# Kernel tuning notes

Measured on AMD Instinct MI355X. Metric: run time of the kernel, lower is better.

Reference implementation:

```python
import jax, jax.numpy as jnp
import numpy as np

B, N, D, H = 32, 64, 128, 256
LN_EPS = 1e-5


def _mlp(x, W1, b1, g, beta, W2, b2):
    # Linear -> LayerNorm -> GELU (exact erf) -> Linear
    h = x @ W1 + b1
    mu = jnp.mean(h, axis=-1, keepdims=True)
    var = jnp.var(h, axis=-1, keepdims=True)
    h = (h - mu) * jax.lax.rsqrt(var + LN_EPS) * g + beta
    h = jax.nn.gelu(h, approximate=False)
    return h @ W2 + b2


def setup_inputs() -> dict:
    key = jax.random.key(0)
    ks = jax.random.split(key, 10)
    s = lambda fan_in: 1.0 / np.sqrt(fan_in)
    return {
        "slots": jax.random.normal(ks[0], (B, N, D), dtype=jnp.float32),
        "adjacency": jax.random.uniform(ks[1], (B, N, N), dtype=jnp.float32),
        # edge_net params
        "We1": jax.random.uniform(ks[2], (2 * D, H), minval=-s(2 * D), maxval=s(2 * D), dtype=jnp.float32),
        "be1": jnp.zeros((H,), jnp.float32),
        "ge": jnp.ones((H,), jnp.float32),
        "bge": jnp.zeros((H,), jnp.float32),
        "We2": jax.random.uniform(ks[3], (H, D), minval=-s(H), maxval=s(H), dtype=jnp.float32),
        "be2": jnp.zeros((D,), jnp.float32),
        # node_net params
        "Wn1": jax.random.uniform(ks[4], (2 * D, H), minval=-s(2 * D), maxval=s(2 * D), dtype=jnp.float32),
        "bn1": jnp.zeros((H,), jnp.float32),
        "gn": jnp.ones((H,), jnp.float32),
        "bgn": jnp.zeros((H,), jnp.float32),
        "Wn2": jax.random.uniform(ks[5], (H, D), minval=-s(H), maxval=s(H), dtype=jnp.float32),
        "bn2": jnp.zeros((D,), jnp.float32),
    }


def reference(slots, adjacency, We1, be1, ge, bge, We2, be2, Wn1, bn1, gn, bgn, Wn2, bn2):
    b, n, d = slots.shape
    # all-pairs edge features: receiver i, sender j -> [B,N,N,2D]
    ei = jnp.broadcast_to(slots[:, :, None, :], (b, n, n, d))
    ej = jnp.broadcast_to(slots[:, None, :, :], (b, n, n, d))
    edge_feat = jnp.concatenate([ei, ej], axis=-1)
    edge_out = _mlp(edge_feat, We1, be1, ge, bge, We2, be2)  # [B,N,N,D]
    # mask diagonal (i != j) and weight by adjacency, then reduce over j
    mask = 1.0 - jnp.eye(n, dtype=slots.dtype)
    w = adjacency * mask  # [B,N,N]
    messages = jnp.einsum('bij,bijd->bid', w, edge_out)
    node_input = jnp.concatenate([slots, messages], axis=-1)
    delta = _mlp(node_input, Wn1, bn1, gn, bgn, Wn2, bn2)
    return slots + delta
```

## Files before the change

### kernel.cpp

```cpp
#include <hip/hip_runtime.h>

#define NB 32
#define NN 64
#define ND 128
#define NH 256
#define LN_EPS 1e-5f
#define RP 4

typedef __attribute__((ext_vector_type(8))) short bf16x8;
typedef __attribute__((ext_vector_type(4))) float f32x4;

__device__ __forceinline__ float gelu2(float x) {
    const float au  = fabsf(x);
    const float xpa = x + au;
    const float z   = au * 0.70710678118654752440f;
    const float z2  = z * z;
    const float pc  = fmaf(0.078108f, z, 0.000972f);
    const float pb  = fmaf(0.278393f, z, 1.0f);
    const float p   = fmaf(z2, fmaf(z, pc, 0.230389f), pb);
    const float p2  = p * p;
    const float r   = __builtin_amdgcn_rcpf(p2 * p2);
    return fmaf(-au, r, xpa);
}
__device__ __forceinline__ float gelu_h(float x) { return 0.5f * gelu2(x); }

__device__ __forceinline__ short f2bf(float f) {
    unsigned u = __float_as_uint(f);
    u += 0x7FFFu + ((u >> 16) & 1u);
    return (short)(u >> 16);
}

__global__ __launch_bounds__(256) void k_pre(const float* __restrict__ slots,
                                             const float* __restrict__ We1,
                                             const float* __restrict__ be1,
                                             const float* __restrict__ Wn1,
                                             const float* __restrict__ We2,
                                             const float* __restrict__ be2,
                                             float* __restrict__ Pt,
                                             float* __restrict__ Qm,
                                             float* __restrict__ XW,
                                             short* __restrict__ Pb,
                                             short* __restrict__ Qb,
                                             float4* __restrict__ rowstats,
                                             float* __restrict__ WC,
                                             float* __restrict__ v) {
    __shared__ float xs[RP][ND];
    __shared__ float red[4][RP][4];
    const int t = threadIdx.x;

    if (blockIdx.x >= 512) {
        const int bid2 = blockIdx.x - 512;
        if (bid2 == 64) {
            __shared__ float bs[ND];
            if (t < ND) bs[t] = be2[t];
            __syncthreads();
            float acc = 0.f;
            #pragma unroll 4
            for (int d = 0; d < ND; ++d) acc = fmaf(bs[d], Wn1[(ND + d) * NH + t], acc);
            v[t] = acc;
            return;
        }
        const int k0 = bid2 * 4;
        __shared__ float ws[4][ND];
        #pragma unroll
        for (int i = 0; i < 2; ++i) {
            const int idx = t + i * 256;
            ws[idx >> 7][idx & 127] = We2[(k0 + (idx >> 7)) * ND + (idx & 127)];
        }
        __syncthreads();
        float acc[4] = {0.f, 0.f, 0.f, 0.f};
        #pragma unroll 4
        for (int d = 0; d < ND; ++d) {
            const float wn = Wn1[(ND + d) * NH + t];
            #pragma unroll
            for (int r = 0; r < 4; ++r) acc[r] = fmaf(ws[r][d], wn, acc[r]);
        }
        #pragma unroll
        for (int r = 0; r < 4; ++r) WC[(k0 + r) * NH + t] = acc[r];
        return;
    }

    const int r0 = blockIdx.x * RP;
    const int lane = t & 63, wave = t >> 6;
    #pragma unroll
    for (int i = 0; i < 2; ++i) {
        const int idx = t + i * 256;
        xs[idx >> 7][idx & 127] = slots[(size_t)(r0 + (idx >> 7)) * ND + (idx & 127)];
    }
    __syncthreads();
    float pt[RP], qq[RP], xw[RP];
    const float bb = be1[t];
    #pragma unroll
    for (int r = 0; r < RP; ++r) { pt[r] = bb; qq[r] = 0.f; xw[r] = 0.f; }
    #pragma unroll 4
    for (int d = 0; d < ND; ++d) {
        const float wt  = We1[d * NH + t];
        const float wbt = We1[(ND + d) * NH + t];
        const float wn  = Wn1[d * NH + t];
        #pragma unroll
        for (int r = 0; r < RP; ++r) {
            const float x = xs[r][d];
            pt[r] = fmaf(x, wt,  pt[r]);
            qq[r] = fmaf(x, wbt, qq[r]);
            xw[r] = fmaf(x, wn,  xw[r]);
        }
    }
    #pragma unroll
    for (int r = 0; r < RP; ++r) {
        const size_t row = (size_t)(r0 + r);
        Pt[row * NH + t] = pt[r];
        Qm[row * NH + t] = qq[r];
        XW[row * NH + t] = xw[r];
        Pb[row * NH + t] = f2bf(pt[r]);
        Qb[row * NH + t] = f2bf(qq[r]);
    }
    float s1[RP], s2[RP], s3[RP], s4[RP];
    #pragma unroll
    for (int r = 0; r < RP; ++r) {
        s1[r] = pt[r]; s2[r] = pt[r] * pt[r];
        s3[r] = qq[r]; s4[r] = qq[r] * qq[r];
    }
    #pragma unroll
    for (int off = 32; off; off >>= 1) {
        #pragma unroll
        for (int r = 0; r < RP; ++r) {
            s1[r] += __shfl_xor(s1[r], off);
            s2[r] += __shfl_xor(s2[r], off);
            s3[r] += __shfl_xor(s3[r], off);
            s4[r] += __shfl_xor(s4[r], off);
        }
    }
    if (lane == 0) {
        #pragma unroll
        for (int r = 0; r < RP; ++r) {
            red[wave][r][0] = s1[r]; red[wave][r][1] = s2[r];
            red[wave][r][2] = s3[r]; red[wave][r][3] = s4[r];
        }
    }
    __syncthreads();
    if (t < RP) {
        float4 st;
        st.x = (red[0][t][0] + red[1][t][0]) + (red[2][t][0] + red[3][t][0]);
        st.y = (red[0][t][1] + red[1][t][1]) + (red[2][t][1] + red[3][t][1]);
        st.z = (red[0][t][2] + red[1][t][2]) + (red[2][t][2] + red[3][t][2]);
        st.w = (red[0][t][3] + red[1][t][3]) + (red[2][t][3] + red[3][t][3]);
        rowstats[r0 + t] = st;
    }
}

__global__ __launch_bounds__(256) void k_dot(
    const short* __restrict__ Pb, const short* __restrict__ Qb,
    const float4* __restrict__ rowstats,
    const float* __restrict__ adj,
    float4* __restrict__ wmrG)
{
    const int b  = blockIdx.x >> 2;
    const int jt = blockIdx.x & 3;
    const int t  = threadIdx.x;
    const int l  = t & 63;
    const int i0 = (t >> 6) * 16;
    const int j0 = jt * 16;
    const int rA = l & 15;
    const int kg = l >> 4;

    const short* Prow = Pb + ((size_t)b * NN + i0 + rA) * NH + kg * 8;
    const short* Qrow = Qb + ((size_t)b * NN + j0 + rA) * NH + kg * 8;
    f32x4 acc = {0.f, 0.f, 0.f, 0.f};
    #pragma unroll
    for (int kc = 0; kc < 8; ++kc) {
        const bf16x8 av = *(const bf16x8*)(Prow + kc * 32);
        const bf16x8 bv = *(const bf16x8*)(Qrow + kc * 32);
        acc = __builtin_amdgcn_mfma_f32_16x16x32_bf16(av, bv, acc, 0, 0, 0);
    }
    const int j  = j0 + (l & 15);
    const int gj = b * NN + j;
    const float4 stj = rowstats[gj];
    const float inv = 1.0f / NH;
    #pragma unroll
    for (int q = 0; q < 4; ++q) {
        const int i  = i0 + (l >> 4) * 4 + q;
        const int gi = b * NN + i;
        const float4 sti = rowstats[gi];
        float a = adj[(size_t)gi * NN + j];
        if (j == i) a = 0.f;
        const float cd = acc[q];
        const float mu = (sti.x + stj.z) * inv;
        const float e2 = fmaf(2.f, cd, sti.y + stj.w) * inv;
        const float rr = __builtin_amdgcn_rsqf(fmaf(-mu, mu, e2) + LN_EPS);
        wmrG[(size_t)gi * NN + j] = make_float4(0.5f * a, rr, -mu * rr, a);
    }
}

__global__ __launch_bounds__(256, 4) void k_mn(
    const float* __restrict__ slots,
    const float* __restrict__ Pt,
    const float* __restrict__ Qm,
    const float4* __restrict__ wmrG,
    const float* __restrict__ ge,  const float* __restrict__ bge,
    const float* __restrict__ XW,
    const float* __restrict__ WC, const float* __restrict__ v,
    const float* __restrict__ bn1,
    const float* __restrict__ gn,  const float* __restrict__ bgn,
    const float* __restrict__ Wn2, const float* __restrict__ bn2,
    float* __restrict__ out)
{
    union U {
        struct { float4 wmr[2][NN]; float s[4][2][NH]; } e;
        struct { float sfg[2][NH];
                 union { float part[2][4][NH]; float d[2][8][ND + 4]; } w; } n;
    };
    __shared__ U u;
    __shared__ float lds_ws[2];
    __shared__ float lds_red[4][2][2];
    __shared__ float lds_mr[2][2];

    const int row0 = blockIdx.x * 2;
    const int b    = row0 >> 6;
    const int t    = threadIdx.x;
    const int lane = t & 63;
    const int wave = t >> 6;

    const float xw0 = XW[(size_t)row0 * NH + t];
    const float xw1 = XW[(size_t)(row0 + 1) * NH + t];
    const float sl  = slots[(size_t)(row0 + (t >> 7)) * ND + (t & 127)];
    if (t < 128) {
        const int r = t >> 6, j = t & 63;
        u.e.wmr[r][j] = wmrG[(size_t)(row0 + r) * NN + j];
    }
    const float4 P0 = ((const float4*)(Pt + (size_t)row0 * NH))[lane];
    const float4 P1 = ((const float4*)(Pt + (size_t)(row0 + 1) * NH))[lane];
    const float4 G  = ((const float4*)ge)[lane];
    const float4 Bg = ((const float4*)bge)[lane];
    __syncthreads();

    if (wave < 2) {
        float wv = u.e.wmr[wave][lane].w;
        #pragma unroll
        for (int off = 32; off; off >>= 1) wv += __shfl_xor(wv, off);
        if (lane == 0) lds_ws[wave] = wv;
    }

    const float4* Qb4 = (const float4*)(Qm + (size_t)b * NN * NH) + lane;
    float4 A0 = make_float4(0.f, 0.f, 0.f, 0.f);
    float4 A1 = make_float4(0.f, 0.f, 0.f, 0.f);
    #pragma unroll 4
    for (int k = 0; k < 16; ++k) {
        const int jj = wave + 4 * k;
        const float4 q  = Qb4[jj * (NH / 4)];
        const float4 m0 = u.e.wmr[0][jj];
        const float4 m1 = u.e.wmr[1][jj];
        float h, uu;
        h = P0.x + q.x; uu = fmaf(fmaf(h, m0.y, m0.z), G.x, Bg.x); A0.x = fmaf(m0.x, gelu2(uu), A0.x);
        h = P0.y + q.y; uu = fmaf(fmaf(h, m0.y, m0.z), G.y, Bg.y); A0.y = fmaf(m0.x, gelu2(uu), A0.y);
        h = P0.z + q.z; uu = fmaf(fmaf(h, m0.y, m0.z), G.z, Bg.z); A0.z = fmaf(m0.x, gelu2(uu), A0.z);
        h = P0.w + q.w; uu = fmaf(fmaf(h, m0.y, m0.z), G.w, Bg.w); A0.w = fmaf(m0.x, gelu2(uu), A0.w);
        h = P1.x + q.x; uu = fmaf(fmaf(h, m1.y, m1.z), G.x, Bg.x); A1.x = fmaf(m1.x, gelu2(uu), A1.x);
        h = P1.y + q.y; uu = fmaf(fmaf(h, m1.y, m1.z), G.y, Bg.y); A1.y = fmaf(m1.x, gelu2(uu), A1.y);
        h = P1.z + q.z; uu = fmaf(fmaf(h, m1.y, m1.z), G.z, Bg.z); A1.z = fmaf(m1.x, gelu2(uu), A1.z);
        h = P1.w + q.w; uu = fmaf(fmaf(h, m1.y, m1.z), G.w, Bg.w); A1.w = fmaf(m1.x, gelu2(uu), A1.w);
    }
    ((float4*)u.e.s[wave][0])[lane] = A0;
    ((float4*)u.e.s[wave][1])[lane] = A1;
    __syncthreads();

    const float sf0 = (u.e.s[0][0][t] + u.e.s[1][0][t]) + (u.e.s[2][0][t] + u.e.s[3][0][t]);
    const float sf1 = (u.e.s[0][1][t] + u.e.s[1][1][t]) + (u.e.s[2][1][t] + u.e.s[3][1][t]);
    u.n.sfg[0][t] = sf0;
    u.n.sfg[1][t] = sf1;
    __syncthreads();

    {
        const int ks = wave;
        const int cg = lane;
        float4 h0 = make_float4(0.f, 0.f, 0.f, 0.f);
        float4 h1 = make_float4(0.f, 0.f, 0.f, 0.f);
        const float4* wc4 = (const float4*)WC + cg;
        #pragma unroll 8
        for (int k = ks * 64; k < ks * 64 + 64; ++k) {
            const float4 w = wc4[k * (NH / 4)];
            const float sa = u.n.sfg[0][k];
            const float sb = u.n.sfg[1][k];
            h0.x = fmaf(sa, w.x, h0.x); h0.y = fmaf(sa, w.y, h0.y);
            h0.z = fmaf(sa, w.z, h0.z); h0.w = fmaf(sa, w.w, h0.w);
            h1.x = fmaf(sb, w.x, h1.x); h1.y = fmaf(sb, w.y, h1.y);
            h1.z = fmaf(sb, w.z, h1.z); h1.w = fmaf(sb, w.w, h1.w);
        }
        ((float4*)u.n.w.part[0][ks])[cg] = h0;
        ((float4*)u.n.w.part[1][ks])[cg] = h1;
    }
    __syncthreads();

    float a0, a1;
    {
        const float b1 = bn1[t], vc = v[t];
        a0 = (u.n.w.part[0][0][t] + u.n.w.part[0][1][t])
           + (u.n.w.part[0][2][t] + u.n.w.part[0][3][t])
           + fmaf(lds_ws[0], vc, b1) + xw0;
        a1 = (u.n.w.part[1][0][t] + u.n.w.part[1][1][t])
           + (u.n.w.part[1][2][t] + u.n.w.part[1][3][t])
           + fmaf(lds_ws[1], vc, b1) + xw1;
    }
    {
        float s1 = a0, s2 = a0 * a0, s3 = a1, s4 = a1 * a1;
        #pragma unroll
        for (int off = 32; off; off >>= 1) {
            s1 += __shfl_xor(s1, off); s2 += __shfl_xor(s2, off);
            s3 += __shfl_xor(s3, off); s4 += __shfl_xor(s4, off);
        }
        if (lane == 0) {
            lds_red[wave][0][0] = s1; lds_red[wave][0][1] = s2;
            lds_red[wave][1][0] = s3; lds_red[wave][1][1] = s4;
        }
    }
    __syncthreads();
    if (t < 2) {
        const float S1 = (lds_red[0][t][0] + lds_red[1][t][0]) + (lds_red[2][t][0] + lds_red[3][t][0]);
        const float S2 = (lds_red[0][t][1] + lds_red[1][t][1]) + (lds_red[2][t][1] + lds_red[3][t][1]);
        const float mu  = S1 * (1.0f / NH);
        const float var = fmaf(-mu, mu, S2 * (1.0f / NH));
        lds_mr[t][0] = mu;
        lds_mr[t][1] = __builtin_amdgcn_rsqf(var + LN_EPS);
    }
    __syncthreads();
    {
        const float g = gn[t], bg = bgn[t];
        const float rr0 = lds_mr[0][1], rr1 = lds_mr[1][1];
        u.n.sfg[0][t] = gelu_h(fmaf(fmaf(a0, rr0, -lds_mr[0][0] * rr0), g, bg));
        u.n.sfg[1][t] = gelu_h(fmaf(fmaf(a1, rr1, -lds_mr[1][0] * rr1), g, bg));
    }
    __syncthreads();

    {
        const int ks = t >> 5;
        const int cg = t & 31;
        float4 d0 = make_float4(0.f, 0.f, 0.f, 0.f);
        float4 d1 = make_float4(0.f, 0.f, 0.f, 0.f);
        const float4* w2 = (const float4*)Wn2 + cg;
        const int kbeg = ks * 32;
        #pragma unroll 8
        for (int k = kbeg; k < kbeg + 32; ++k) {
            const float4 w = w2[k * (ND / 4)];
            const float g0 = u.n.sfg[0][k];
            const float g1 = u.n.sfg[1][k];
            d0.x = fmaf(g0, w.x, d0.x); d0.y = fmaf(g0, w.y, d0.y);
            d0.z = fmaf(g0, w.z, d0.z); d0.w = fmaf(g0, w.w, d0.w);
            d1.x = fmaf(g1, w.x, d1.x); d1.y = fmaf(g1, w.y, d1.y);
            d1.z = fmaf(g1, w.z, d1.z); d1.w = fmaf(g1, w.w, d1.w);
        }
        ((float4*)u.n.w.d[0][ks])[cg] = d0;
        ((float4*)u.n.w.d[1][ks])[cg] = d1;
    }
    __syncthreads();
    {
        const int r  = t >> 7;
        const int c2 = t & 127;
        float ds = 0.f;
        #pragma unroll
        for (int p2 = 0; p2 < 8; ++p2) ds += u.n.w.d[r][p2][c2];
        out[(size_t)(row0 + r) * ND + c2] = sl + bn2[c2] + ds;
    }
}

extern "C" void kernel_launch(void* const* d_in, const int* in_sizes, int n_in,
                              void* d_out, int out_size, void* d_ws, size_t ws_size,
                              hipStream_t stream) {
    const float* slots = (const float*)d_in[0];
    const float* adj   = (const float*)d_in[1];
    const float* We1   = (const float*)d_in[2];
    const float* be1   = (const float*)d_in[3];
    const float* ge    = (const float*)d_in[4];
    const float* bge   = (const float*)d_in[5];
    const float* We2   = (const float*)d_in[6];
    const float* be2   = (const float*)d_in[7];
    const float* Wn1   = (const float*)d_in[8];
    const float* bn1   = (const float*)d_in[9];
    const float* gn    = (const float*)d_in[10];
    const float* bgn   = (const float*)d_in[11];
    const float* Wn2   = (const float*)d_in[12];
    const float* bn2   = (const float*)d_in[13];
    float* out = (float*)d_out;

    const size_t RN = (size_t)NB * NN;
    float*  Ptw  = (float*)d_ws;
    float*  Qw   = Ptw  + RN * NH;
    float*  XWw  = Qw   + RN * NH;
    float*  WCw  = XWw  + RN * NH;
    float*  vw   = WCw  + (size_t)NH * NH;
    float4* rsw  = (float4*)(vw + NH);
    float4* wmrw = rsw + RN;
    short*  Pbw  = (short*)(wmrw + RN * NN);
    short*  Qbw  = Pbw + RN * NH;

    k_pre<<<577,           256, 0, stream>>>(slots, We1, be1, Wn1, We2, be2,
                                             Ptw, Qw, XWw, Pbw, Qbw, rsw, WCw, vw);
    k_dot<<<NB * 4,        256, 0, stream>>>(Pbw, Qbw, rsw, adj, wmrw);
    k_mn <<<(int)(RN / 2), 256, 0, stream>>>(slots, Ptw, Qw, wmrw, ge, bge,
                                             XWw, WCw, vw, bn1, gn, bgn, Wn2, bn2, out);
}
```

Before: 56.98 us.

## Split message and node MLP into separate kernels using bf16 MFMA for node GEMMs

The fused k_mn kernel becomes two kernels. k_msg handles one row per block and computes the GELU-weighted edge message sums, writing them as bf16. k_node processes 16 rows per block and runs both node-MLP matmuls (WC and Wn2) with bf16 16x16x32 MFMA instead of scalar FMA loops, with a cross-row LayerNorm done in LDS. k_pre gains extra blocks that write WC and Wn2 as transposed bf16 weights. This adds a kernel launch and a global round-trip for the message sums, and lowers the node-MLP matmul inputs to bf16 precision.

```diff
diff --git a/kernel.cpp b/kernel.cpp
--- a/kernel.cpp
+++ b/kernel.cpp
@@ -36,14 +36,16 @@
                                              const float* __restrict__ Wn1,
                                              const float* __restrict__ We2,
                                              const float* __restrict__ be2,
+                                             const float* __restrict__ Wn2,
                                              float* __restrict__ Pt,
                                              float* __restrict__ Qm,
                                              float* __restrict__ XW,
                                              short* __restrict__ Pb,
                                              short* __restrict__ Qb,
                                              float4* __restrict__ rowstats,
-                                             float* __restrict__ WC,
-                                             float* __restrict__ v) {
+                                             short* __restrict__ WCbT,
+                                             float* __restrict__ v,
+                                             short* __restrict__ Wn2bT) {
     __shared__ float xs[RP][ND];
     __shared__ float red[4][RP][4];
     const int t = threadIdx.x;
@@ -60,6 +62,14 @@
             v[t] = acc;
             return;
         }
+        if (bid2 > 64) {
+            const int c0 = (bid2 - 65) * 32;
+            for (int ci = 0; ci < 32; ++ci) {
+                const int c = c0 + ci;
+                Wn2bT[(size_t)c * NH + t] = f2bf(Wn2[(size_t)t * ND + c]);
+            }
+            return;
+        }
         const int k0 = bid2 * 4;
         __shared__ float ws[4][ND];
         #pragma unroll
@@ -75,8 +85,10 @@
             #pragma unroll
             for (int r = 0; r < 4; ++r) acc[r] = fmaf(ws[r][d], wn, acc[r]);
         }
-        #pragma unroll
-        for (int r = 0; r < 4; ++r) WC[(k0 + r) * NH + t] = acc[r];
+        short4 pk;
+        pk.x = f2bf(acc[0]); pk.y = f2bf(acc[1]);
+        pk.z = f2bf(acc[2]); pk.w = f2bf(acc[3]);
+        *(short4*)(WCbT + (size_t)t * NH + k0) = pk;
         return;
     }
 
@@ -172,13 +184,13 @@
         const bf16x8 bv = *(const bf16x8*)(Qrow + kc * 32);
         acc = __builtin_amdgcn_mfma_f32_16x16x32_bf16(av, bv, acc, 0, 0, 0);
     }
-    const int j  = j0 + (l & 15);
+    const int j  = j0 + rA;
     const int gj = b * NN + j;
     const float4 stj = rowstats[gj];
     const float inv = 1.0f / NH;
     #pragma unroll
     for (int q = 0; q < 4; ++q) {
-        const int i  = i0 + (l >> 4) * 4 + q;
+        const int i  = i0 + kg * 4 + q;
         const int gi = b * NN + i;
         const float4 sti = rowstats[gi];
         float a = adj[(size_t)gi * NN + j];
@@ -191,131 +203,124 @@
     }
 }
 
-__global__ __launch_bounds__(256, 4) void k_mn(
-    const float* __restrict__ slots,
+__global__ __launch_bounds__(256, 8) void k_msg(
     const float* __restrict__ Pt,
     const float* __restrict__ Qm,
     const float4* __restrict__ wmrG,
     const float* __restrict__ ge,  const float* __restrict__ bge,
-    const float* __restrict__ XW,
-    const float* __restrict__ WC, const float* __restrict__ v,
-    const float* __restrict__ bn1,
-    const float* __restrict__ gn,  const float* __restrict__ bgn,
-    const float* __restrict__ Wn2, const float* __restrict__ bn2,
-    float* __restrict__ out)
+    short* __restrict__ Sb, float* __restrict__ wsumw)
 {
-    union U {
-        struct { float4 wmr[2][NN]; float s[4][2][NH]; } e;
-        struct { float sfg[2][NH];
-                 union { float part[2][4][NH]; float d[2][8][ND + 4]; } w; } n;
-    };
-    __shared__ U u;
-    __shared__ float lds_ws[2];
-    __shared__ float lds_red[4][2][2];
-    __shared__ float lds_mr[2][2];
-
-    const int row0 = blockIdx.x * 2;
-    const int b    = row0 >> 6;
-    const int t    = threadIdx.x;
+    __shared__ float4 wmr[NN];
+    __shared__ float  s[4][NH];
+
+    const int row = blockIdx.x;
+    const int b   = row >> 6;
+    const int t   = threadIdx.x;
     const int lane = t & 63;
     const int wave = t >> 6;
 
-    const float xw0 = XW[(size_t)row0 * NH + t];
-    const float xw1 = XW[(size_t)(row0 + 1) * NH + t];
-    const float sl  = slots[(size_t)(row0 + (t >> 7)) * ND + (t & 127)];
-    if (t < 128) {
-        const int r = t >> 6, j = t & 63;
-        u.e.wmr[r][j] = wmrG[(size_t)(row0 + r) * NN + j];
-    }
-    const float4 P0 = ((const float4*)(Pt + (size_t)row0 * NH))[lane];
-    const float4 P1 = ((const float4*)(Pt + (size_t)(row0 + 1) * NH))[lane];
+    if (t < NN) wmr[t] = wmrG[(size_t)row * NN + t];
+    const float4 P  = ((const float4*)(Pt + (size_t)row * NH))[lane];
     const float4 G  = ((const float4*)ge)[lane];
     const float4 Bg = ((const float4*)bge)[lane];
     __syncthreads();
 
-    if (wave < 2) {
-        float wv = u.e.wmr[wave][lane].w;
+    if (wave == 0) {
+        float wv = wmr[lane].w;
         #pragma unroll
         for (int off = 32; off; off >>= 1) wv += __shfl_xor(wv, off);
-        if (lane == 0) lds_ws[wave] = wv;
+        if (lane == 0) wsumw[row] = wv;
     }
 
     const float4* Qb4 = (const float4*)(Qm + (size_t)b * NN * NH) + lane;
-    float4 A0 = make_float4(0.f, 0.f, 0.f, 0.f);
-    float4 A1 = make_float4(0.f, 0.f, 0.f, 0.f);
+    float4 A = make_float4(0.f, 0.f, 0.f, 0.f);
     #pragma unroll 4
     for (int k = 0; k < 16; ++k) {
         const int jj = wave + 4 * k;
-        const float4 q  = Qb4[jj * (NH / 4)];
-        const float4 m0 = u.e.wmr[0][jj];
-        const float4 m1 = u.e.wmr[1][jj];
+        const float4 q = Qb4[jj * (NH / 4)];
+        const float4 m = wmr[jj];
         float h, uu;
-        h = P0.x + q.x; uu = fmaf(fmaf(h, m0.y, m0.z), G.x, Bg.x); A0.x = fmaf(m0.x, gelu2(uu), A0.x);
-        h = P0.y + q.y; uu = fmaf(fmaf(h, m0.y, m0.z), G.y, Bg.y); A0.y = fmaf(m0.x, gelu2(uu), A0.y);
-        h = P0.z + q.z; uu = fmaf(fmaf(h, m0.y, m0.z), G.z, Bg.z); A0.z = fmaf(m0.x, gelu2(uu), A0.z);
-        h = P0.w + q.w; uu = fmaf(fmaf(h, m0.y, m0.z), G.w, Bg.w); A0.w = fmaf(m0.x, gelu2(uu), A0.w);
-        h = P1.x + q.x; uu = fmaf(fmaf(h, m1.y, m1.z), G.x, Bg.x); A1.x = fmaf(m1.x, gelu2(uu), A1.x);
-        h = P1.y + q.y; uu = fmaf(fmaf(h, m1.y, m1.z), G.y, Bg.y); A1.y = fmaf(m1.x, gelu2(uu), A1.y);
-        h = P1.z + q.z; uu = fmaf(fmaf(h, m1.y, m1.z), G.z, Bg.z); A1.z = fmaf(m1.x, gelu2(uu), A1.z);
-        h = P1.w + q.w; uu = fmaf(fmaf(h, m1.y, m1.z), G.w, Bg.w); A1.w = fmaf(m1.x, gelu2(uu), A1.w);
-    }
-    ((float4*)u.e.s[wave][0])[lane] = A0;
-    ((float4*)u.e.s[wave][1])[lane] = A1;
-    __syncthreads();
-
-    const float sf0 = (u.e.s[0][0][t] + u.e.s[1][0][t]) + (u.e.s[2][0][t] + u.e.s[3][0][t]);
-    const float sf1 = (u.e.s[0][1][t] + u.e.s[1][1][t]) + (u.e.s[2][1][t] + u.e.s[3][1][t]);
-    u.n.sfg[0][t] = sf0;
-    u.n.sfg[1][t] = sf1;
-    __syncthreads();
-
+        h = P.x + q.x; uu = fmaf(fmaf(h, m.y, m.z), G.x, Bg.x); A.x = fmaf(m.x, gelu2(uu), A.x);
+        h = P.y + q.y; uu = fmaf(fmaf(h, m.y, m.z), G.y, Bg.y); A.y = fmaf(m.x, gelu2(uu), A.y);
+        h = P.z + q.z; uu = fmaf(fmaf(h, m.y, m.z), G.z, Bg.z); A.z = fmaf(m.x, gelu2(uu), A.z);
+        h = P.w + q.w; uu = fmaf(fmaf(h, m.y, m.z), G.w, Bg.w); A.w = fmaf(m.x, gelu2(uu), A.w);
+    }
+    ((float4*)s[wave])[lane] = A;
+    __syncthreads();
+    const float Sf = (s[0][t] + s[1][t]) + (s[2][t] + s[3][t]);
+    Sb[(size_t)row * NH + t] = f2bf(Sf);
+}
+
+#define HS 261
+__global__ __launch_bounds__(256) void k_node(
+    const float* __restrict__ slots,
+    const short* __restrict__ Sb,
+    const float* __restrict__ wsumw,
+    const float* __restrict__ XW,
+    const short* __restrict__ WCbT,
+    const float* __restrict__ v,
+    const float* __restrict__ bn1,
+    const float* __restrict__ gn,  const float* __restrict__ bgn,
+    const short* __restrict__ Wn2bT,
+    const float* __restrict__ bn2,
+    float* __restrict__ out)
+{
+    __shared__ float lds_h[16][HS];
+    __shared__ short lds_g[16][264];
+    __shared__ float red1[16][16], red2[16][16];
+    __shared__ float lds_mr[16][2];
+
+    const int r0 = blockIdx.x * 16;
+    const int t  = threadIdx.x;
+    const int l  = t & 63;
+    const int w  = t >> 6;
+    const int rA = l & 15;
+    const int kg = l >> 4;
+    const int orow = kg * 4;
+
+    bf16x8 afr[8];
     {
-        const int ks = wave;
-        const int cg = lane;
-        float4 h0 = make_float4(0.f, 0.f, 0.f, 0.f);
-        float4 h1 = make_float4(0.f, 0.f, 0.f, 0.f);
-        const float4* wc4 = (const float4*)WC + cg;
-        #pragma unroll 8
-        for (int k = ks * 64; k < ks * 64 + 64; ++k) {
-            const float4 w = wc4[k * (NH / 4)];
-            const float sa = u.n.sfg[0][k];
-            const float sb = u.n.sfg[1][k];
-            h0.x = fmaf(sa, w.x, h0.x); h0.y = fmaf(sa, w.y, h0.y);
-            h0.z = fmaf(sa, w.z, h0.z); h0.w = fmaf(sa, w.w, h0.w);
-            h1.x = fmaf(sb, w.x, h1.x); h1.y = fmaf(sb, w.y, h1.y);
-            h1.z = fmaf(sb, w.z, h1.z); h1.w = fmaf(sb, w.w, h1.w);
-        }
-        ((float4*)u.n.w.part[0][ks])[cg] = h0;
-        ((float4*)u.n.w.part[1][ks])[cg] = h1;
-    }
-    __syncthreads();
-
-    float a0, a1;
+        const short* Arow = Sb + (size_t)(r0 + rA) * NH + kg * 8;
+        #pragma unroll
+        for (int kc = 0; kc < 8; ++kc) afr[kc] = *(const bf16x8*)(Arow + kc * 32);
+    }
+
+    #pragma unroll
+    for (int cti = 0; cti < 4; ++cti) {
+        const int ct = w * 4 + cti;
+        const short* Brow = WCbT + (size_t)(ct * 16 + rA) * NH + kg * 8;
+        f32x4 acc = {0.f, 0.f, 0.f, 0.f};
+        #pragma unroll
+        for (int kc = 0; kc < 8; ++kc) {
+            const bf16x8 bv = *(const bf16x8*)(Brow + kc * 32);
+            acc = __builtin_amdgcn_mfma_f32_16x16x32_bf16(afr[kc], bv, acc, 0, 0, 0);
+        }
+        const int col = ct * 16 + rA;
+        const float vc = v[col], b1 = bn1[col];
+        #pragma unroll
+        for (int q = 0; q < 4; ++q) {
+            const int row = orow + q;
+            lds_h[row][col] = acc[q] + XW[(size_t)(r0 + row) * NH + col]
+                            + fmaf(wsumw[r0 + row], vc, b1);
+        }
+    }
+    __syncthreads();
+
     {
-        const float b1 = bn1[t], vc = v[t];
-        a0 = (u.n.w.part[0][0][t] + u.n.w.part[0][1][t])
-           + (u.n.w.part[0][2][t] + u.n.w.part[0][3][t])
-           + fmaf(lds_ws[0], vc, b1) + xw0;
-        a1 = (u.n.w.part[1][0][t] + u.n.w.part[1][1][t])
-           + (u.n.w.part[1][2][t] + u.n.w.part[1][3][t])
-           + fmaf(lds_ws[1], vc, b1) + xw1;
-    }
-    {
-        float s1 = a0, s2 = a0 * a0, s3 = a1, s4 = a1 * a1;
-        #pragma unroll
-        for (int off = 32; off; off >>= 1) {
-            s1 += __shfl_xor(s1, off); s2 += __shfl_xor(s2, off);
-            s3 += __shfl_xor(s3, off); s4 += __shfl_xor(s4, off);
-        }
-        if (lane == 0) {
-            lds_red[wave][0][0] = s1; lds_red[wave][0][1] = s2;
-            lds_red[wave][1][0] = s3; lds_red[wave][1][1] = s4;
-        }
-    }
-    __syncthreads();
-    if (t < 2) {
-        const float S1 = (lds_red[0][t][0] + lds_red[1][t][0]) + (lds_red[2][t][0] + lds_red[3][t][0]);
-        const float S2 = (lds_red[0][t][1] + lds_red[1][t][1]) + (lds_red[2][t][1] + lds_red[3][t][1]);
+        const int row = t & 15, grp = t >> 4;
+        float s1 = 0.f, s2 = 0.f;
+        #pragma unroll
+        for (int c = grp * 16; c < grp * 16 + 16; ++c) {
+            const float h = lds_h[row][c];
+            s1 += h; s2 = fmaf(h, h, s2);
+        }
+        red1[row][grp] = s1; red2[row][grp] = s2;
+    }
+    __syncthreads();
+    if (t < 16) {
+        float S1 = 0.f, S2 = 0.f;
+        #pragma unroll
+        for (int g = 0; g < 16; ++g) { S1 += red1[t][g]; S2 += red2[t][g]; }
         const float mu  = S1 * (1.0f / NH);
         const float var = fmaf(-mu, mu, S2 * (1.0f / NH));
         lds_mr[t][0] = mu;
@@ -323,41 +328,35 @@
     }
     __syncthreads();
     {
-        const float g = gn[t], bg = bgn[t];
-        const float rr0 = lds_mr[0][1], rr1 = lds_mr[1][1];
-        u.n.sfg[0][t] = gelu_h(fmaf(fmaf(a0, rr0, -lds_mr[0][0] * rr0), g, bg));
-        u.n.sfg[1][t] = gelu_h(fmaf(fmaf(a1, rr1, -lds_mr[1][0] * rr1), g, bg));
-    }
-    __syncthreads();
-
-    {
-        const int ks = t >> 5;
-        const int cg = t & 31;
-        float4 d0 = make_float4(0.f, 0.f, 0.f, 0.f);
-        float4 d1 = make_float4(0.f, 0.f, 0.f, 0.f);
-        const float4* w2 = (const float4*)Wn2 + cg;
-        const int kbeg = ks * 32;
-        #pragma unroll 8
-        for (int k = kbeg; k < kbeg + 32; ++k) {
-            const float4 w = w2[k * (ND / 4)];
-            const float g0 = u.n.sfg[0][k];
-            const float g1 = u.n.sfg[1][k];
-            d0.x = fmaf(g0, w.x, d0.x); d0.y = fmaf(g0, w.y, d0.y);
-            d0.z = fmaf(g0, w.z, d0.z); d0.w = fmaf(g0, w.w, d0.w);
-            d1.x = fmaf(g1, w.x, d1.x); d1.y = fmaf(g1, w.y, d1.y);
-            d1.z = fmaf(g1, w.z, d1.z); d1.w = fmaf(g1, w.w, d1.w);
-        }
-        ((float4*)u.n.w.d[0][ks])[cg] = d0;
-        ((float4*)u.n.w.d[1][ks])[cg] = d1;
-    }
-    __syncthreads();
-    {
-        const int r  = t >> 7;
-        const int c2 = t & 127;
-        float ds = 0.f;
-        #pragma unroll
-        for (int p2 = 0; p2 < 8; ++p2) ds += u.n.w.d[r][p2][c2];
-        out[(size_t)(row0 + r) * ND + c2] = sl + bn2[c2] + ds;
+        const float gc = gn[t], bgc = bgn[t];
+        #pragma unroll
+        for (int r = 0; r < 16; ++r) {
+            const float rr = lds_mr[r][1];
+            const float u0 = fmaf(lds_h[r][t], rr, -lds_mr[r][0] * rr);
+            lds_g[r][t] = f2bf(gelu_h(fmaf(u0, gc, bgc)));
+        }
+    }
+    __syncthreads();
+
+    #pragma unroll
+    for (int cti = 0; cti < 2; ++cti) {
+        const int ct = w * 2 + cti;
+        const short* Brow = Wn2bT + (size_t)(ct * 16 + rA) * NH + kg * 8;
+        f32x4 acc = {0.f, 0.f, 0.f, 0.f};
+        #pragma unroll
+        for (int kc = 0; kc < 8; ++kc) {
+            const bf16x8 av = *(const bf16x8*)(&lds_g[rA][kg * 8 + kc * 32]);
+            const bf16x8 bv = *(const bf16x8*)(Brow + kc * 32);
+            acc = __builtin_amdgcn_mfma_f32_16x16x32_bf16(av, bv, acc, 0, 0, 0);
+        }
+        const int col = ct * 16 + rA;
+        const float b2 = bn2[col];
+        #pragma unroll
+        for (int q = 0; q < 4; ++q) {
+            const int row = orow + q;
+            const size_t o = (size_t)(r0 + row) * ND + col;
+            out[o] = slots[o] + b2 + acc[q];
+        }
     }
 }
 
@@ -381,19 +380,23 @@
     float* out = (float*)d_out;
 
     const size_t RN = (size_t)NB * NN;
-    float*  Ptw  = (float*)d_ws;
-    float*  Qw   = Ptw  + RN * NH;
-    float*  XWw  = Qw   + RN * NH;
-    float*  WCw  = XWw  + RN * NH;
-    float*  vw   = WCw  + (size_t)NH * NH;
-    float4* rsw  = (float4*)(vw + NH);
-    float4* wmrw = rsw + RN;
-    short*  Pbw  = (short*)(wmrw + RN * NN);
-    short*  Qbw  = Pbw + RN * NH;
-
-    k_pre<<<577,           256, 0, stream>>>(slots, We1, be1, Wn1, We2, be2,
-                                             Ptw, Qw, XWw, Pbw, Qbw, rsw, WCw, vw);
-    k_dot<<<NB * 4,        256, 0, stream>>>(Pbw, Qbw, rsw, adj, wmrw);
-    k_mn <<<(int)(RN / 2), 256, 0, stream>>>(slots, Ptw, Qw, wmrw, ge, bge,
-                                             XWw, WCw, vw, bn1, gn, bgn, Wn2, bn2, out);
-}
+    float*  Ptw    = (float*)d_ws;
+    float*  Qw     = Ptw  + RN * NH;
+    float*  XWw    = Qw   + RN * NH;
+    float*  vw     = XWw  + RN * NH;
+    float*  wsumw  = vw   + NH;
+    float4* rsw    = (float4*)(wsumw + RN);
+    float4* wmrw   = rsw + RN;
+    short*  Pbw    = (short*)(wmrw + RN * NN);
+    short*  Qbw    = Pbw  + RN * NH;
+    short*  Sbw    = Qbw  + RN * NH;
+    short*  WCbTw  = Sbw  + RN * NH;
+    short*  Wn2bTw = WCbTw + (size_t)NH * NH;
+
+    k_pre <<<581,             256, 0, stream>>>(slots, We1, be1, Wn1, We2, be2, Wn2,
+                                                Ptw, Qw, XWw, Pbw, Qbw, rsw, WCbTw, vw, Wn2bTw);
+    k_dot <<<NB * 4,          256, 0, stream>>>(Pbw, Qbw, rsw, adj, wmrw);
+    k_msg <<<(int)RN,         256, 0, stream>>>(Ptw, Qw, wmrw, ge, bge, Sbw, wsumw);
+    k_node<<<(int)(RN / 16),  256, 0, stream>>>(slots, Sbw, wsumw, XWw, WCbTw, vw,
+                                                bn1, gn, bgn, Wn2bTw, bn2, out);
+}
```

Result: slower. 63.25 us (+11.0%).

## Move slot projections onto bf16 MFMA with pre-transposed bf16 weights

Applied to the files above, without the earlier changes.

Splits the old k_pre into a weight-prep kernel (WC, v, and a transposed bf16 copy of We1/Wn1) and a new k_pmm kernel that computes P, Q and XW for 16 rows per block with bf16 MFMA instead of scalar fp32 FMAs. Row statistics are reduced through LDS. This cuts the FMA-bound projection cost but adds an extra kernel launch and a weight conversion pass on every call. It also lowers P/Q/XW accuracy to bf16-input precision. An extra barrier is inserted in k_mn before the union LDS reuse.

```diff
diff --git a/kernel.cpp b/kernel.cpp
--- a/kernel.cpp
+++ b/kernel.cpp
@@ -5,7 +5,6 @@
 #define ND 128
 #define NH 256
 #define LN_EPS 1e-5f
-#define RP 4
 
 typedef __attribute__((ext_vector_type(8))) short bf16x8;
 typedef __attribute__((ext_vector_type(4))) float f32x4;
@@ -30,37 +29,17 @@
     return (short)(u >> 16);
 }
 
-__global__ __launch_bounds__(256) void k_pre(const float* __restrict__ slots,
-                                             const float* __restrict__ We1,
-                                             const float* __restrict__ be1,
-                                             const float* __restrict__ Wn1,
-                                             const float* __restrict__ We2,
-                                             const float* __restrict__ be2,
-                                             float* __restrict__ Pt,
-                                             float* __restrict__ Qm,
-                                             float* __restrict__ XW,
-                                             short* __restrict__ Pb,
-                                             short* __restrict__ Qb,
-                                             float4* __restrict__ rowstats,
-                                             float* __restrict__ WC,
-                                             float* __restrict__ v) {
-    __shared__ float xs[RP][ND];
-    __shared__ float red[4][RP][4];
+__global__ __launch_bounds__(256) void k_prep(const float* __restrict__ We1,
+                                              const float* __restrict__ Wn1,
+                                              const float* __restrict__ We2,
+                                              const float* __restrict__ be2,
+                                              float* __restrict__ WC,
+                                              float* __restrict__ v,
+                                              short* __restrict__ WT) {
     const int t = threadIdx.x;
-
-    if (blockIdx.x >= 512) {
-        const int bid2 = blockIdx.x - 512;
-        if (bid2 == 64) {
-            __shared__ float bs[ND];
-            if (t < ND) bs[t] = be2[t];
-            __syncthreads();
-            float acc = 0.f;
-            #pragma unroll 4
-            for (int d = 0; d < ND; ++d) acc = fmaf(bs[d], Wn1[(ND + d) * NH + t], acc);
-            v[t] = acc;
-            return;
-        }
-        const int k0 = bid2 * 4;
+    const int bid = blockIdx.x;
+    if (bid < 64) {
+        const int k0 = bid * 4;
         __shared__ float ws[4][ND];
         #pragma unroll
         for (int i = 0; i < 2; ++i) {
@@ -79,72 +58,116 @@
         for (int r = 0; r < 4; ++r) WC[(k0 + r) * NH + t] = acc[r];
         return;
     }
-
-    const int r0 = blockIdx.x * RP;
-    const int lane = t & 63, wave = t >> 6;
+    if (bid == 64) {
+        __shared__ float bs[ND];
+        if (t < ND) bs[t] = be2[t];
+        __syncthreads();
+        float acc = 0.f;
+        #pragma unroll 4
+        for (int d = 0; d < ND; ++d) acc = fmaf(bs[d], Wn1[(ND + d) * NH + t], acc);
+        v[t] = acc;
+        return;
+    }
+    const int r   = bid - 65;
+    const int m   = r >> 3;
+    const int c0  = (r & 7) * 32;
+    const int col = c0 + (t & 31);
+    const int d0  = (t >> 5) * 16;
+    const float* src = (m == 0) ? We1 : (m == 1) ? (We1 + ND * NH) : Wn1;
+    short* dst = WT + ((size_t)m * NH + col) * ND + d0;
+    #pragma unroll 4
+    for (int i = 0; i < 16; ++i)
+        dst[i] = f2bf(src[(size_t)(d0 + i) * NH + col]);
+}
+
+__global__ __launch_bounds__(256) void k_pmm(const float* __restrict__ slots,
+                                             const float* __restrict__ be1,
+                                             const short* __restrict__ WT,
+                                             float* __restrict__ Pt,
+                                             float* __restrict__ Qm,
+                                             float* __restrict__ XW,
+                                             short* __restrict__ Pb,
+                                             short* __restrict__ Qb,
+                                             float4* __restrict__ rowstats) {
+    __shared__ float lds_h[16][264];
+    __shared__ float red1[16][16], red2[16][16];
+    __shared__ float stP1[16], stP2[16], stQ1[16], stQ2[16];
+
+    const int r0 = blockIdx.x * 16;
+    const int t  = threadIdx.x;
+    const int l  = t & 63;
+    const int w  = t >> 6;
+    const int rA = l & 15;
+    const int kg = l >> 4;
+
+    bf16x8 afr[4];
+    {
+        const float* srow = slots + (size_t)(r0 + rA) * ND + kg * 8;
+        #pragma unroll
+        for (int kc = 0; kc < 4; ++kc) {
+            const float4 a = *(const float4*)(srow + kc * 32);
+            const float4 b = *(const float4*)(srow + kc * 32 + 4);
+            bf16x8 cv;
+            cv[0] = f2bf(a.x); cv[1] = f2bf(a.y); cv[2] = f2bf(a.z); cv[3] = f2bf(a.w);
+            cv[4] = f2bf(b.x); cv[5] = f2bf(b.y); cv[6] = f2bf(b.z); cv[7] = f2bf(b.w);
+            afr[kc] = cv;
+        }
+    }
+
+    const int srow_stat = t & 15, grp = t >> 4;
+
     #pragma unroll
-    for (int i = 0; i < 2; ++i) {
-        const int idx = t + i * 256;
-        xs[idx >> 7][idx & 127] = slots[(size_t)(r0 + (idx >> 7)) * ND + (idx & 127)];
-    }
-    __syncthreads();
-    float pt[RP], qq[RP], xw[RP];
-    const float bb = be1[t];
-    #pragma unroll
-    for (int r = 0; r < RP; ++r) { pt[r] = bb; qq[r] = 0.f; xw[r] = 0.f; }
-    #pragma unroll 4
-    for (int d = 0; d < ND; ++d) {
-        const float wt  = We1[d * NH + t];
-        const float wbt = We1[(ND + d) * NH + t];
-        const float wn  = Wn1[d * NH + t];
-        #pragma unroll
-        for (int r = 0; r < RP; ++r) {
-            const float x = xs[r][d];
-            pt[r] = fmaf(x, wt,  pt[r]);
-            qq[r] = fmaf(x, wbt, qq[r]);
-            xw[r] = fmaf(x, wn,  xw[r]);
-        }
-    }
-    #pragma unroll
-    for (int r = 0; r < RP; ++r) {
-        const size_t row = (size_t)(r0 + r);
-        Pt[row * NH + t] = pt[r];
-        Qm[row * NH + t] = qq[r];
-        XW[row * NH + t] = xw[r];
-        Pb[row * NH + t] = f2bf(pt[r]);
-        Qb[row * NH + t] = f2bf(qq[r]);
-    }
-    float s1[RP], s2[RP], s3[RP], s4[RP];
-    #pragma unroll
-    for (int r = 0; r < RP; ++r) {
-        s1[r] = pt[r]; s2[r] = pt[r] * pt[r];
-        s3[r] = qq[r]; s4[r] = qq[r] * qq[r];
-    }
-    #pragma unroll
-    for (int off = 32; off; off >>= 1) {
-        #pragma unroll
-        for (int r = 0; r < RP; ++r) {
-            s1[r] += __shfl_xor(s1[r], off);
-            s2[r] += __shfl_xor(s2[r], off);
-            s3[r] += __shfl_xor(s3[r], off);
-            s4[r] += __shfl_xor(s4[r], off);
-        }
-    }
-    if (lane == 0) {
-        #pragma unroll
-        for (int r = 0; r < RP; ++r) {
-            red[wave][r][0] = s1[r]; red[wave][r][1] = s2[r];
-            red[wave][r][2] = s3[r]; red[wave][r][3] = s4[r];
-        }
-    }
-    __syncthreads();
-    if (t < RP) {
-        float4 st;
-        st.x = (red[0][t][0] + red[1][t][0]) + (red[2][t][0] + red[3][t][0]);
-        st.y = (red[0][t][1] + red[1][t][1]) + (red[2][t][1] + red[3][t][1]);
-        st.z = (red[0][t][2] + red[1][t][2]) + (red[2][t][2] + red[3][t][2]);
-        st.w = (red[0][t][3] + red[1][t][3]) + (red[2][t][3] + red[3][t][3]);
-        rowstats[r0 + t] = st;
+    for (int m = 0; m < 3; ++m) {
+        if (m) __syncthreads();
+        #pragma unroll
+        for (int cti = 0; cti < 4; ++cti) {
+            const int ct = w * 4 + cti;
+            const short* Brow = WT + ((size_t)m * NH + ct * 16 + rA) * ND + kg * 8;
+            f32x4 acc = {0.f, 0.f, 0.f, 0.f};
+            #pragma unroll
+            for (int kc = 0; kc < 4; ++kc) {
+                const bf16x8 bv = *(const bf16x8*)(Brow + kc * 32);
+                acc = __builtin_amdgcn_mfma_f32_16x16x32_bf16(afr[kc], bv, acc, 0, 0, 0);
+            }
+            const int col = ct * 16 + rA;
+            const float add = (m == 0) ? be1[col] : 0.f;
+            #pragma unroll
+            for (int q = 0; q < 4; ++q)
+                lds_h[kg * 4 + q][col] = acc[q] + add;
+        }
+        __syncthreads();
+
+        if (m < 2) {
+            float* Fo = (m == 0) ? Pt : Qm;
+            short* Bo = (m == 0) ? Pb : Qb;
+            #pragma unroll 4
+            for (int r = 0; r < 16; ++r) {
+                const float val = lds_h[r][t];
+                Fo[(size_t)(r0 + r) * NH + t] = val;
+                Bo[(size_t)(r0 + r) * NH + t] = f2bf(val);
+            }
+            float s1 = 0.f, s2 = 0.f;
+            #pragma unroll
+            for (int c = grp * 16; c < grp * 16 + 16; ++c) {
+                const float h = lds_h[srow_stat][c];
+                s1 += h; s2 = fmaf(h, h, s2);
+            }
+            red1[srow_stat][grp] = s1; red2[srow_stat][grp] = s2;
+            __syncthreads();
+            if (t < 16) {
+                float S1 = 0.f, S2 = 0.f;
+                #pragma unroll
+                for (int g = 0; g < 16; ++g) { S1 += red1[t][g]; S2 += red2[t][g]; }
+                if (m == 0) { stP1[t] = S1; stP2[t] = S2; }
+                else        { stQ1[t] = S1; stQ2[t] = S2; }
+            }
+        } else {
+            #pragma unroll 4
+            for (int r = 0; r < 16; ++r)
+                XW[(size_t)(r0 + r) * NH + t] = lds_h[r][t];
+            if (t < 16)
+                rowstats[r0 + t] = make_float4(stP1[t], stP2[t], stQ1[t], stQ2[t]);
+        }
     }
 }
 
@@ -172,13 +195,13 @@
         const bf16x8 bv = *(const bf16x8*)(Qrow + kc * 32);
         acc = __builtin_amdgcn_mfma_f32_16x16x32_bf16(av, bv, acc, 0, 0, 0);
     }
-    const int j  = j0 + (l & 15);
+    const int j  = j0 + rA;
     const int gj = b * NN + j;
     const float4 stj = rowstats[gj];
     const float inv = 1.0f / NH;
     #pragma unroll
     for (int q = 0; q < 4; ++q) {
-        const int i  = i0 + (l >> 4) * 4 + q;
+        const int i  = i0 + kg * 4 + q;
         const int gi = b * NN + i;
         const float4 sti = rowstats[gi];
         float a = adj[(size_t)gi * NN + j];
@@ -265,6 +288,7 @@
 
     const float sf0 = (u.e.s[0][0][t] + u.e.s[1][0][t]) + (u.e.s[2][0][t] + u.e.s[3][0][t]);
     const float sf1 = (u.e.s[0][1][t] + u.e.s[1][1][t]) + (u.e.s[2][1][t] + u.e.s[3][1][t]);
+    __syncthreads();
     u.n.sfg[0][t] = sf0;
     u.n.sfg[1][t] = sf1;
     __syncthreads();
@@ -277,13 +301,13 @@
         const float4* wc4 = (const float4*)WC + cg;
         #pragma unroll 8
         for (int k = ks * 64; k < ks * 64 + 64; ++k) {
-            const float4 w = wc4[k * (NH / 4)];
+            const float4 wv = wc4[k * (NH / 4)];
             const float sa = u.n.sfg[0][k];
             const float sb = u.n.sfg[1][k];
-            h0.x = fmaf(sa, w.x, h0.x); h0.y = fmaf(sa, w.y, h0.y);
-            h0.z = fmaf(sa, w.z, h0.z); h0.w = fmaf(sa, w.w, h0.w);
-            h1.x = fmaf(sb, w.x, h1.x); h1.y = fmaf(sb, w.y, h1.y);
-            h1.z = fmaf(sb, w.z, h1.z); h1.w = fmaf(sb, w.w, h1.w);
+            h0.x = fmaf(sa, wv.x, h0.x); h0.y = fmaf(sa, wv.y, h0.y);
+            h0.z = fmaf(sa, wv.z, h0.z); h0.w = fmaf(sa, wv.w, h0.w);
+            h1.x = fmaf(sb, wv.x, h1.x); h1.y = fmaf(sb, wv.y, h1.y);
+            h1.z = fmaf(sb, wv.z, h1.z); h1.w = fmaf(sb, wv.w, h1.w);
         }
         ((float4*)u.n.w.part[0][ks])[cg] = h0;
         ((float4*)u.n.w.part[1][ks])[cg] = h1;
@@ -339,13 +363,13 @@
         const int kbeg = ks * 32;
         #pragma unroll 8
         for (int k = kbeg; k < kbeg + 32; ++k) {
-            const float4 w = w2[k * (ND / 4)];
+            const float4 wv = w2[k * (ND / 4)];
             const float g0 = u.n.sfg[0][k];
             const float g1 = u.n.sfg[1][k];
-            d0.x = fmaf(g0, w.x, d0.x); d0.y = fmaf(g0, w.y, d0.y);
-            d0.z = fmaf(g0, w.z, d0.z); d0.w = fmaf(g0, w.w, d0.w);
-            d1.x = fmaf(g1, w.x, d1.x); d1.y = fmaf(g1, w.y, d1.y);
-            d1.z = fmaf(g1, w.z, d1.z); d1.w = fmaf(g1, w.w, d1.w);
+            d0.x = fmaf(g0, wv.x, d0.x); d0.y = fmaf(g0, wv.y, d0.y);
+            d0.z = fmaf(g0, wv.z, d0.z); d0.w = fmaf(g0, wv.w, d0.w);
+            d1.x = fmaf(g1, wv.x, d1.x); d1.y = fmaf(g1, wv.y, d1.y);
+            d1.z = fmaf(g1, wv.z, d1.z); d1.w = fmaf(g1, wv.w, d1.w);
         }
         ((float4*)u.n.w.d[0][ks])[cg] = d0;
         ((float4*)u.n.w.d[1][ks])[cg] = d1;
@@ -390,10 +414,11 @@
     float4* wmrw = rsw + RN;
     short*  Pbw  = (short*)(wmrw + RN * NN);
     short*  Qbw  = Pbw + RN * NH;
-
-    k_pre<<<577,           256, 0, stream>>>(slots, We1, be1, Wn1, We2, be2,
-                                             Ptw, Qw, XWw, Pbw, Qbw, rsw, WCw, vw);
-    k_dot<<<NB * 4,        256, 0, stream>>>(Pbw, Qbw, rsw, adj, wmrw);
-    k_mn <<<(int)(RN / 2), 256, 0, stream>>>(slots, Ptw, Qw, wmrw, ge, bge,
-                                             XWw, WCw, vw, bn1, gn, bgn, Wn2, bn2, out);
-}
+    short*  WTw  = Qbw + RN * NH;
+
+    k_prep<<<89,             256, 0, stream>>>(We1, Wn1, We2, be2, WCw, vw, WTw);
+    k_pmm <<<(int)(RN / 16), 256, 0, stream>>>(slots, be1, WTw, Ptw, Qw, XWw, Pbw, Qbw, rsw);
+    k_dot <<<NB * 4,         256, 0, stream>>>(Pbw, Qbw, rsw, adj, wmrw);
+    k_mn  <<<(int)(RN / 2),  256, 0, stream>>>(slots, Ptw, Qw, wmrw, ge, bge,
+                                               XWw, WCw, vw, bn1, gn, bgn, Wn2, bn2, out);
+}
```

Result: slower. 60.27 us (+5.8%).
